# Kernel optimization log

Hardware: AMD Instinct MI355X
Metric: run time of the kernel (lower is better)

Reference implementation:

```python
import jax, jax.numpy as jnp
import numpy as np

B, S, D, H = 2, 2048, 1024, 16
DK = D // H

def setup_inputs() -> dict:
    key = jax.random.key(0)
    ks = jax.random.split(key, 12)
    def lin(k, shape, fan_in):
        bound = 1.0 / np.sqrt(fan_in)
        return jax.random.uniform(k, shape, jnp.float32, -bound, bound)
    inp = {
        'Q': jax.random.normal(ks[0], (B, S, D), jnp.float32),
        'K': jax.random.normal(ks[1], (B, S, D), jnp.float32),
        'V': jax.random.normal(ks[2], (B, S, D), jnp.float32),
        # padding mask: last 128 key positions of batch element 0 are padding
        'padding_mask': jnp.ones((B, 1, 1, S), jnp.int32).at[0, :, :, -128:].set(0),
        # causal look-ahead mask
        'look_ahead_mask': jnp.tril(jnp.ones((S, S), jnp.int32))[None, None],
        'Wq': lin(ks[3], (D, D), D), 'bq': lin(ks[4], (D,), D),
        'Wk': lin(ks[5], (D, D), D), 'bk': lin(ks[6], (D,), D),
        'Wv': lin(ks[7], (D, D), D), 'bv': lin(ks[8], (D,), D),
        'Wo': lin(ks[9], (D, D), D), 'bo': lin(ks[10], (D,), D),
    }
    return inp

def _split_heads(x):
    # [B,S,D] -> [B,H,S,DK]
    b, s, _ = x.shape
    return x.reshape(b, s, H, DK).transpose(0, 2, 1, 3)

def reference(Q, K, V, padding_mask, look_ahead_mask, Wq, bq, Wk, bk, Wv, bv, Wo, bo):
    q = _split_heads(Q @ Wq.T + bq)  # [B,H,S,DK]
    k = _split_heads(K @ Wk.T + bk)
    v = _split_heads(V @ Wv.T + bv)
    scores = jnp.einsum('bhqd,bhkd->bhqk', q, k) / np.sqrt(DK).astype(np.float32)
    neg_inf = jnp.float32(-jnp.inf)
    scores = jnp.where(padding_mask == 0, neg_inf, scores)
    scores = jnp.where(look_ahead_mask == 0, neg_inf, scores)
    weights = jax.nn.softmax(scores, axis=-1)  # dropout is identity in eval mode
    x = jnp.einsum('bhqk,bhkd->bhqd', weights, v)  # [B,H,S,DK]
    x = x.transpose(0, 2, 1, 3).reshape(Q.shape[0], Q.shape[1], D)
    return x @ Wo.T + bo
```

## Files before the change

kernel.cpp:

```cpp
#include <hip/hip_runtime.h>
#include <hip/hip_bf16.h>

#define B_   2
#define S_   2048
#define D_   1024
#define H_   16
#define DK_  64

typedef unsigned short u16;
typedef __attribute__((ext_vector_type(8))) short bf16x8;
typedef __attribute__((ext_vector_type(4))) float f32x4;

static __device__ __forceinline__ u16 f2bf(float f) {
  union { float f; unsigned u; } v; v.f = f;
  unsigned r = v.u + 0x7FFF + ((v.u >> 16) & 1);
  return (u16)(r >> 16);
}

static __device__ __forceinline__ void gl_lds16(const void* g, void* l) {
  __builtin_amdgcn_global_load_lds(
      (const __attribute__((address_space(1))) void*)g,
      (__attribute__((address_space(3))) void*)l, 16, 0, 0);
}

__global__ void cvt3(const float4* __restrict__ a, const float4* __restrict__ b, const float4* __restrict__ c,
                     ushort4* __restrict__ oa, ushort4* __restrict__ ob, ushort4* __restrict__ oc, int n4) {
  int y = blockIdx.y;
  const float4* in = (y == 0) ? a : (y == 1) ? b : c;
  ushort4* out = (y == 0) ? oa : (y == 1) ? ob : oc;
  int i = blockIdx.x * blockDim.x + threadIdx.x;
  if (i < n4) {
    float4 v = in[i];
    ushort4 r;
    r.x = f2bf(v.x); r.y = f2bf(v.y); r.z = f2bf(v.z); r.w = f2bf(v.w);
    out[i] = r;
  }
}
__global__ void cvt4(const float4* __restrict__ a, const float4* __restrict__ b, const float4* __restrict__ c,
                     const float4* __restrict__ d, ushort4* __restrict__ oa, ushort4* __restrict__ ob,
                     ushort4* __restrict__ oc, ushort4* __restrict__ od, int n4) {
  int y = blockIdx.y;
  const float4* in = (y == 0) ? a : (y == 1) ? b : (y == 2) ? c : d;
  ushort4* out = (y == 0) ? oa : (y == 1) ? ob : (y == 2) ? oc : od;
  int i = blockIdx.x * blockDim.x + threadIdx.x;
  if (i < n4) {
    float4 v = in[i];
    ushort4 r;
    r.x = f2bf(v.x); r.y = f2bf(v.y); r.z = f2bf(v.z); r.w = f2bf(v.w);
    out[i] = r;
  }
}

__launch_bounds__(256, 2)
__global__ void gemm_qkv(const u16* __restrict__ Xq, const u16* __restrict__ Xk, const u16* __restrict__ Xv,
                         const u16* __restrict__ Wq, const u16* __restrict__ Wk, const u16* __restrict__ Wv,
                         const float* __restrict__ bq, const float* __restrict__ bk, const float* __restrict__ bv,
                         u16* __restrict__ outq, u16* __restrict__ outk, u16* __restrict__ outv) {
  const int z = blockIdx.z;
  const u16* Am; const u16* Bm; int m0, n0;
  if (z == 2) { Am = Wv; Bm = Xv; m0 = blockIdx.x * 128; n0 = blockIdx.y * 128; }
  else if (z == 1) { Am = Xk; Bm = Wk; m0 = blockIdx.y * 128; n0 = blockIdx.x * 128; }
  else { Am = Xq; Bm = Wq; m0 = blockIdx.y * 128; n0 = blockIdx.x * 128; }
  const float* bias = (z == 0) ? bq : (z == 1) ? bk : bv;

  __shared__ __align__(16) u16 As[128 * 32];
  __shared__ __align__(16) u16 Bs[128 * 32];

  const int tid = threadIdx.x, lane = tid & 63, w = tid >> 6;
  const int q = lane >> 4, cl = lane & 15;
  const int wr = w >> 1, wc = w & 1;

  f32x4 acc[4][4] = {};

  for (int k0 = 0; k0 < D_; k0 += 32) {
#pragma unroll
    for (int i = 0; i < 2; ++i) {
      int cb = (i * 4 + w) * 64;
      int ch = cb + lane;
      int row = ch >> 2, ko = (ch & 3) << 3;
      gl_lds16(Am + (size_t)(m0 + row) * D_ + k0 + ko, As + cb * 8);
      gl_lds16(Bm + (size_t)(n0 + row) * D_ + k0 + ko, Bs + cb * 8);
    }
    __syncthreads();

    bf16x8 af[4], bfr[4];
#pragma unroll
    for (int r = 0; r < 4; ++r) af[r]  = *(const bf16x8*)(As + (wr * 64 + r * 16 + cl) * 32 + q * 8);
#pragma unroll
    for (int c = 0; c < 4; ++c) bfr[c] = *(const bf16x8*)(Bs + (wc * 64 + c * 16 + cl) * 32 + q * 8);
#pragma unroll
    for (int r = 0; r < 4; ++r)
#pragma unroll
      for (int c = 0; c < 4; ++c)
        acc[r][c] = __builtin_amdgcn_mfma_f32_16x16x32_bf16(af[r], bfr[c], acc[r][c], 0, 0, 0);
    __syncthreads();
  }

  if (z == 2) {
#pragma unroll
    for (int r = 0; r < 4; ++r) {
#pragma unroll
      for (int rr = 0; rr < 4; ++rr) {
        int j = m0 + wr * 64 + r * 16 + q * 4 + rr;
        float bval = bias[j];
        int hh = j >> 6, dk = j & 63;
#pragma unroll
        for (int c = 0; c < 4; ++c) {
          int n = n0 + wc * 64 + c * 16 + cl;
          int bb = n >> 11, s = n & (S_ - 1);
          outv[((size_t)(bb * H_ + hh) * DK_ + dk) * S_ + s] = f2bf(acc[r][c][rr] + bval);
        }
      }
    }
  } else {
    const float scale = (z == 0) ? 0.125f : 1.0f;
    u16* o = (z == 0) ? outq : outk;
#pragma unroll
    for (int c = 0; c < 4; ++c) {
      int j = n0 + wc * 64 + c * 16 + cl;
      float bval = bias[j];
      int hh = j >> 6, dk = j & 63;
#pragma unroll
      for (int r = 0; r < 4; ++r) {
#pragma unroll
        for (int rr = 0; rr < 4; ++rr) {
          int n = m0 + wr * 64 + r * 16 + q * 4 + rr;
          int bb = n >> 11, s = n & (S_ - 1);
          o[((size_t)(bb * H_ + hh) * S_ + s) * DK_ + dk] = f2bf((acc[r][c][rr] + bval) * scale);
        }
      }
    }
  }
}

__launch_bounds__(256, 2)
__global__ void attn(const u16* __restrict__ qh, const u16* __restrict__ kh,
                     const u16* __restrict__ vt, const int* __restrict__ pad,
                     u16* __restrict__ attn_out) {
  __shared__ __align__(16) u16 Ks[64 * 64];
  __shared__ __align__(16) u16 Vs[64 * 64];
  __shared__ __align__(16) u16 Ps[4][16 * 72];
  __shared__ float Kbias[64];

  const int tid = threadIdx.x, lane = tid & 63, w = tid >> 6;
  const int q = lane >> 4, cl = lane & 15;
  const int qt = (int)gridDim.x - 1 - (int)blockIdx.x;
  const int qb = qt * 64, h = blockIdx.y, b = blockIdx.z;

  const u16* Q = qh + (size_t)(b * H_ + h) * S_ * DK_;
  const u16* K = kh + (size_t)(b * H_ + h) * S_ * DK_;
  const u16* V = vt + (size_t)(b * H_ + h) * DK_ * S_;
  const int* pm = pad + b * S_;

  const int qr0 = qb + w * 16;
  bf16x8 qf0 = *(const bf16x8*)(Q + (qr0 + cl) * DK_ + q * 8);
  bf16x8 qf1 = *(const bf16x8*)(Q + (qr0 + cl) * DK_ + 32 + q * 8);

  f32x4 o[4] = {};
  float ls[4] = {0.f, 0.f, 0.f, 0.f};
  u16* Pw = Ps[w];

  const int nkv = qt + 1;
  for (int it = 0; it < nkv; ++it) {
    const int kb = it << 6;
#pragma unroll
    for (int i = 0; i < 2; ++i) {
      int s = (i * 4 + w) * 64 + lane;
      int row = s >> 3;
      int c = (s & 7) ^ (row & 7);
      gl_lds16(K + (size_t)(kb + row) * DK_ + (c << 3), Ks + (size_t)s * 8);
      gl_lds16(V + (size_t)row * S_ + kb + (c << 3), Vs + (size_t)s * 8);
    }
    if (tid < 64) {
      Kbias[tid] = (pm[kb + tid] != 0) ? -6.0f : -3e38f;
    }
    __syncthreads();

    f32x4 sa[4];
#pragma unroll
    for (int ct = 0; ct < 4; ++ct) {
      int rk = ct * 16 + cl;
      int c0 = q ^ (rk & 7);
      bf16x8 kf0 = *(const bf16x8*)(Ks + rk * 64 + (c0 << 3));
      bf16x8 kf1 = *(const bf16x8*)(Ks + rk * 64 + ((c0 ^ 4) << 3));
      f32x4 zz = {};
      zz = __builtin_amdgcn_mfma_f32_16x16x32_bf16(qf0, kf0, zz, 0, 0, 0);
      zz = __builtin_amdgcn_mfma_f32_16x16x32_bf16(qf1, kf1, zz, 0, 0, 0);
      sa[ct] = zz;
    }

    if (it < qt) {
#pragma unroll
      for (int ct = 0; ct < 4; ++ct) {
        float kbv = Kbias[ct * 16 + cl];
#pragma unroll
        for (int rr = 0; rr < 4; ++rr) {
          float p = __expf(sa[ct][rr] + kbv);
          ls[rr] += p;
          Pw[(q * 4 + rr) * 72 + ct * 16 + cl] = f2bf(p);
        }
      }
    } else {
#pragma unroll
      for (int ct = 0; ct < 4; ++ct) {
        int kg = kb + ct * 16 + cl;
        float kbv = Kbias[ct * 16 + cl];
#pragma unroll
        for (int rr = 0; rr < 4; ++rr) {
          int qg = qr0 + q * 4 + rr;
          float p = (kg <= qg) ? __expf(sa[ct][rr] + kbv) : 0.f;
          ls[rr] += p;
          Pw[(q * 4 + rr) * 72 + ct * 16 + cl] = f2bf(p);
        }
      }
    }

    bf16x8 pf0 = *(const bf16x8*)(Pw + cl * 72 + q * 8);
    bf16x8 pf1 = *(const bf16x8*)(Pw + cl * 72 + 32 + q * 8);

#pragma unroll
    for (int ct = 0; ct < 4; ++ct) {
      int rv = ct * 16 + cl;
      int c0 = q ^ (rv & 7);
      bf16x8 vf0 = *(const bf16x8*)(Vs + rv * 64 + (c0 << 3));
      bf16x8 vf1 = *(const bf16x8*)(Vs + rv * 64 + ((c0 ^ 4) << 3));
      o[ct] = __builtin_amdgcn_mfma_f32_16x16x32_bf16(pf0, vf0, o[ct], 0, 0, 0);
      o[ct] = __builtin_amdgcn_mfma_f32_16x16x32_bf16(pf1, vf1, o[ct], 0, 0, 0);
    }
    __syncthreads();
  }

#pragma unroll
  for (int rr = 0; rr < 4; ++rr) {
    float l = ls[rr];
    l += __shfl_xor(l, 1, 64);
    l += __shfl_xor(l, 2, 64);
    l += __shfl_xor(l, 4, 64);
    l += __shfl_xor(l, 8, 64);
    float inv = 1.0f / l;
    int qg = qr0 + q * 4 + rr;
    size_t base = (size_t)(b * S_ + qg) * D_ + h * DK_;
#pragma unroll
    for (int ct = 0; ct < 4; ++ct)
      attn_out[base + ct * 16 + cl] = f2bf(o[ct][rr] * inv);
  }
}

__launch_bounds__(256, 2)
__global__ void gemm_out(const u16* __restrict__ A, const u16* __restrict__ W,
                         const float* __restrict__ bias, float* __restrict__ out) {
  __shared__ __align__(16) u16 As[128 * 32];
  __shared__ __align__(16) u16 Bs[128 * 32];

  const int tid = threadIdx.x, lane = tid & 63, w = tid >> 6;
  const int q = lane >> 4, cl = lane & 15;
  const int wr = w >> 1, wc = w & 1;
  const int m0 = blockIdx.y * 128, n0 = blockIdx.x * 128;

  f32x4 acc[4][4] = {};

  for (int k0 = 0; k0 < D_; k0 += 32) {
#pragma unroll
    for (int i = 0; i < 2; ++i) {
      int cb = (i * 4 + w) * 64;
      int ch = cb + lane;
      int row = ch >> 2, ko = (ch & 3) << 3;
      gl_lds16(A + (size_t)(m0 + row) * D_ + k0 + ko, As + cb * 8);
      gl_lds16(W + (size_t)(n0 + row) * D_ + k0 + ko, Bs + cb * 8);
    }
    __syncthreads();

    bf16x8 af[4], bfr[4];
#pragma unroll
    for (int r = 0; r < 4; ++r) af[r]  = *(const bf16x8*)(As + (wr * 64 + r * 16 + cl) * 32 + q * 8);
#pragma unroll
    for (int c = 0; c < 4; ++c) bfr[c] = *(const bf16x8*)(Bs + (wc * 64 + c * 16 + cl) * 32 + q * 8);
#pragma unroll
    for (int r = 0; r < 4; ++r)
#pragma unroll
      for (int c = 0; c < 4; ++c)
        acc[r][c] = __builtin_amdgcn_mfma_f32_16x16x32_bf16(af[r], bfr[c], acc[r][c], 0, 0, 0);
    __syncthreads();
  }

#pragma unroll
  for (int c = 0; c < 4; ++c) {
    int j = n0 + wc * 64 + c * 16 + cl;
    float bval = bias[j];
#pragma unroll
    for (int r = 0; r < 4; ++r) {
#pragma unroll
      for (int rr = 0; rr < 4; ++rr) {
        int n = m0 + wr * 64 + r * 16 + q * 4 + rr;
        out[(size_t)n * D_ + j] = acc[r][c][rr] + bval;
      }
    }
  }
}

extern "C" void kernel_launch(void* const* d_in, const int* in_sizes, int n_in,
                              void* d_out, int out_size, void* d_ws, size_t ws_size,
                              hipStream_t stream) {
  const float* Qf  = (const float*)d_in[0];
  const float* Kf  = (const float*)d_in[1];
  const float* Vf  = (const float*)d_in[2];
  const int*   pad = (const int*)d_in[3];
  const float* Wqf = (const float*)d_in[5];
  const float* bq  = (const float*)d_in[6];
  const float* Wkf = (const float*)d_in[7];
  const float* bk  = (const float*)d_in[8];
  const float* Wvf = (const float*)d_in[9];
  const float* bv  = (const float*)d_in[10];
  const float* Wof = (const float*)d_in[11];
  const float* bo  = (const float*)d_in[12];

  const size_t BSD = (size_t)B_ * S_ * D_;
  const size_t DD  = (size_t)D_ * D_;

  char* ws = (char*)d_ws;
  u16* Qb   = (u16*)ws; ws += BSD * 2;
  u16* Kb   = (u16*)ws; ws += BSD * 2;
  u16* Vb   = (u16*)ws; ws += BSD * 2;
  u16* Wqb  = (u16*)ws; ws += DD * 2;
  u16* Wkb  = (u16*)ws; ws += DD * 2;
  u16* Wvb  = (u16*)ws; ws += DD * 2;
  u16* Wob  = (u16*)ws; ws += DD * 2;
  u16* qhd  = (u16*)ws; ws += BSD * 2;
  u16* khd  = (u16*)ws; ws += BSD * 2;
  u16* vtd  = (u16*)ws; ws += BSD * 2;
  u16* attn_o = (u16*)ws; ws += BSD * 2;

  const int n4 = (int)(BSD / 4);
  const int w4 = (int)(DD / 4);
  dim3 gc3(n4 / 256, 3), gc4(w4 / 256, 4);
  cvt3<<<gc3, 256, 0, stream>>>((const float4*)Qf, (const float4*)Kf, (const float4*)Vf,
                                (ushort4*)Qb, (ushort4*)Kb, (ushort4*)Vb, n4);
  cvt4<<<gc4, 256, 0, stream>>>((const float4*)Wqf, (const float4*)Wkf, (const float4*)Wvf, (const float4*)Wof,
                                (ushort4*)Wqb, (ushort4*)Wkb, (ushort4*)Wvb, (ushort4*)Wob, w4);

  dim3 g1(D_ / 128, (B_ * S_) / 128, 3);
  gemm_qkv<<<g1, 256, 0, stream>>>(Qb, Kb, Vb, Wqb, Wkb, Wvb, bq, bk, bv, qhd, khd, vtd);

  dim3 g2(S_ / 64, H_, B_);
  attn<<<g2, 256, 0, stream>>>(qhd, khd, vtd, pad, attn_o);

  dim3 g3(D_ / 128, (B_ * S_) / 128);
  gemm_out<<<g3, 256, 0, stream>>>(attn_o, Wob, bo, (float*)d_out);
}
```

Baseline: 258.5 us.

## Load K/V fragments directly from global memory, dropping LDS staging and barriers

```diff
diff --git a/kernel.cpp b/kernel.cpp
--- a/kernel.cpp
+++ b/kernel.cpp
@@ -133,14 +133,11 @@
   }
 }
 
-__launch_bounds__(256, 2)
+__launch_bounds__(256, 4)
 __global__ void attn(const u16* __restrict__ qh, const u16* __restrict__ kh,
                      const u16* __restrict__ vt, const int* __restrict__ pad,
                      u16* __restrict__ attn_out) {
-  __shared__ __align__(16) u16 Ks[64 * 64];
-  __shared__ __align__(16) u16 Vs[64 * 64];
   __shared__ __align__(16) u16 Ps[4][16 * 72];
-  __shared__ float Kbias[64];
 
   const int tid = threadIdx.x, lane = tid & 63, w = tid >> 6;
   const int q = lane >> 4, cl = lane & 15;
@@ -163,26 +160,18 @@
   const int nkv = qt + 1;
   for (int it = 0; it < nkv; ++it) {
     const int kb = it << 6;
-#pragma unroll
-    for (int i = 0; i < 2; ++i) {
-      int s = (i * 4 + w) * 64 + lane;
-      int row = s >> 3;
-      int c = (s & 7) ^ (row & 7);
-      gl_lds16(K + (size_t)(kb + row) * DK_ + (c << 3), Ks + (size_t)s * 8);
-      gl_lds16(V + (size_t)row * S_ + kb + (c << 3), Vs + (size_t)s * 8);
-    }
-    if (tid < 64) {
-      Kbias[tid] = (pm[kb + tid] != 0) ? -6.0f : -3e38f;
-    }
-    __syncthreads();
+
+    float kbv[4];
+#pragma unroll
+    for (int ct = 0; ct < 4; ++ct)
+      kbv[ct] = (pm[kb + ct * 16 + cl] != 0) ? -6.0f : -3e38f;
 
     f32x4 sa[4];
 #pragma unroll
     for (int ct = 0; ct < 4; ++ct) {
-      int rk = ct * 16 + cl;
-      int c0 = q ^ (rk & 7);
-      bf16x8 kf0 = *(const bf16x8*)(Ks + rk * 64 + (c0 << 3));
-      bf16x8 kf1 = *(const bf16x8*)(Ks + rk * 64 + ((c0 ^ 4) << 3));
+      const u16* Kr = K + (size_t)(kb + ct * 16 + cl) * DK_;
+      bf16x8 kf0 = *(const bf16x8*)(Kr + q * 8);
+      bf16x8 kf1 = *(const bf16x8*)(Kr + 32 + q * 8);
       f32x4 zz = {};
       zz = __builtin_amdgcn_mfma_f32_16x16x32_bf16(qf0, kf0, zz, 0, 0, 0);
       zz = __builtin_amdgcn_mfma_f32_16x16x32_bf16(qf1, kf1, zz, 0, 0, 0);
@@ -192,10 +181,9 @@
     if (it < qt) {
 #pragma unroll
       for (int ct = 0; ct < 4; ++ct) {
-        float kbv = Kbias[ct * 16 + cl];
 #pragma unroll
         for (int rr = 0; rr < 4; ++rr) {
-          float p = __expf(sa[ct][rr] + kbv);
+          float p = __expf(sa[ct][rr] + kbv[ct]);
           ls[rr] += p;
           Pw[(q * 4 + rr) * 72 + ct * 16 + cl] = f2bf(p);
         }
@@ -204,11 +192,10 @@
 #pragma unroll
       for (int ct = 0; ct < 4; ++ct) {
         int kg = kb + ct * 16 + cl;
-        float kbv = Kbias[ct * 16 + cl];
 #pragma unroll
         for (int rr = 0; rr < 4; ++rr) {
           int qg = qr0 + q * 4 + rr;
-          float p = (kg <= qg) ? __expf(sa[ct][rr] + kbv) : 0.f;
+          float p = (kg <= qg) ? __expf(sa[ct][rr] + kbv[ct]) : 0.f;
           ls[rr] += p;
           Pw[(q * 4 + rr) * 72 + ct * 16 + cl] = f2bf(p);
         }
@@ -220,14 +207,12 @@
 
 #pragma unroll
     for (int ct = 0; ct < 4; ++ct) {
-      int rv = ct * 16 + cl;
-      int c0 = q ^ (rv & 7);
-      bf16x8 vf0 = *(const bf16x8*)(Vs + rv * 64 + (c0 << 3));
-      bf16x8 vf1 = *(const bf16x8*)(Vs + rv * 64 + ((c0 ^ 4) << 3));
+      const u16* Vr = V + (size_t)(ct * 16 + cl) * S_ + kb;
+      bf16x8 vf0 = *(const bf16x8*)(Vr + q * 8);
+      bf16x8 vf1 = *(const bf16x8*)(Vr + 32 + q * 8);
       o[ct] = __builtin_amdgcn_mfma_f32_16x16x32_bf16(pf0, vf0, o[ct], 0, 0, 0);
       o[ct] = __builtin_amdgcn_mfma_f32_16x16x32_bf16(pf1, vf1, o[ct], 0, 0, 0);
     }
-    __syncthreads();
   }
 
 #pragma unroll
```

New measurement: 428.2 us. +65.6%, slower.

## Split long causal KV ranges into chunks with a separate combine kernel

Applied to the files above, without the earlier changes.

```diff
diff --git a/kernel.cpp b/kernel.cpp
--- a/kernel.cpp
+++ b/kernel.cpp
@@ -11,6 +11,9 @@
 typedef __attribute__((ext_vector_type(8))) short bf16x8;
 typedef __attribute__((ext_vector_type(4))) float f32x4;
 
+#define CHUNK_   12
+#define NSLOT_   48
+
 static __device__ __forceinline__ u16 f2bf(float f) {
   union { float f; unsigned u; } v; v.f = f;
   unsigned r = v.u + 0x7FFF + ((v.u >> 16) & 1);
@@ -23,27 +26,27 @@
       (__attribute__((address_space(3))) void*)l, 16, 0, 0);
 }
 
-__global__ void cvt3(const float4* __restrict__ a, const float4* __restrict__ b, const float4* __restrict__ c,
-                     ushort4* __restrict__ oa, ushort4* __restrict__ ob, ushort4* __restrict__ oc, int n4) {
+__global__ void cvt7(const float4* __restrict__ i0, const float4* __restrict__ i1,
+                     const float4* __restrict__ i2, const float4* __restrict__ i3,
+                     const float4* __restrict__ i4, const float4* __restrict__ i5,
+                     const float4* __restrict__ i6,
+                     ushort4* __restrict__ o0, ushort4* __restrict__ o1,
+                     ushort4* __restrict__ o2, ushort4* __restrict__ o3,
+                     ushort4* __restrict__ o4, ushort4* __restrict__ o5,
+                     ushort4* __restrict__ o6, int nbig, int nsmall) {
   int y = blockIdx.y;
-  const float4* in = (y == 0) ? a : (y == 1) ? b : c;
-  ushort4* out = (y == 0) ? oa : (y == 1) ? ob : oc;
+  const float4* in; ushort4* out; int bound;
+  switch (y) {
+    case 0: in = i0; out = o0; bound = nbig; break;
+    case 1: in = i1; out = o1; bound = nbig; break;
+    case 2: in = i2; out = o2; bound = nbig; break;
+    case 3: in = i3; out = o3; bound = nsmall; break;
+    case 4: in = i4; out = o4; bound = nsmall; break;
+    case 5: in = i5; out = o5; bound = nsmall; break;
+    default: in = i6; out = o6; bound = nsmall; break;
+  }
   int i = blockIdx.x * blockDim.x + threadIdx.x;
-  if (i < n4) {
-    float4 v = in[i];
-    ushort4 r;
-    r.x = f2bf(v.x); r.y = f2bf(v.y); r.z = f2bf(v.z); r.w = f2bf(v.w);
-    out[i] = r;
-  }
-}
-__global__ void cvt4(const float4* __restrict__ a, const float4* __restrict__ b, const float4* __restrict__ c,
-                     const float4* __restrict__ d, ushort4* __restrict__ oa, ushort4* __restrict__ ob,
-                     ushort4* __restrict__ oc, ushort4* __restrict__ od, int n4) {
-  int y = blockIdx.y;
-  const float4* in = (y == 0) ? a : (y == 1) ? b : (y == 2) ? c : d;
-  ushort4* out = (y == 0) ? oa : (y == 1) ? ob : (y == 2) ? oc : od;
-  int i = blockIdx.x * blockDim.x + threadIdx.x;
-  if (i < n4) {
+  if (i < bound) {
     float4 v = in[i];
     ushort4 r;
     r.x = f2bf(v.x); r.y = f2bf(v.y); r.z = f2bf(v.z); r.w = f2bf(v.w);
@@ -133,10 +136,10 @@
   }
 }
 
-__launch_bounds__(256, 2)
+__launch_bounds__(256, 4)
 __global__ void attn(const u16* __restrict__ qh, const u16* __restrict__ kh,
                      const u16* __restrict__ vt, const int* __restrict__ pad,
-                     u16* __restrict__ attn_out) {
+                     u16* __restrict__ attn_out, float* __restrict__ Po, float* __restrict__ Pl) {
   __shared__ __align__(16) u16 Ks[64 * 64];
   __shared__ __align__(16) u16 Vs[64 * 64];
   __shared__ __align__(16) u16 Ps[4][16 * 72];
@@ -144,8 +147,16 @@
 
   const int tid = threadIdx.x, lane = tid & 63, w = tid >> 6;
   const int q = lane >> 4, cl = lane & 15;
-  const int qt = (int)gridDim.x - 1 - (int)blockIdx.x;
-  const int qb = qt * 64, h = blockIdx.y, b = blockIdx.z;
+  const int h = blockIdx.y, b = blockIdx.z;
+
+  const int x = blockIdx.x;
+  int qt, ch, nch;
+  if (x < 24)      { qt = 24 + x / 3;          ch = x % 3;       nch = 3; }
+  else if (x < 48) { int y = x - 24; qt = 12 + y / 2; ch = y & 1; nch = 2; }
+  else             { qt = x - 48;              ch = 0;           nch = 1; }
+  const int qb = qt * 64;
+  const int t0 = ch * CHUNK_;
+  const int t1 = (qt < t0 + CHUNK_ - 1) ? qt : (t0 + CHUNK_ - 1);
 
   const u16* Q = qh + (size_t)(b * H_ + h) * S_ * DK_;
   const u16* K = kh + (size_t)(b * H_ + h) * S_ * DK_;
@@ -160,8 +171,7 @@
   float ls[4] = {0.f, 0.f, 0.f, 0.f};
   u16* Pw = Ps[w];
 
-  const int nkv = qt + 1;
-  for (int it = 0; it < nkv; ++it) {
+  for (int it = t0; it <= t1; ++it) {
     const int kb = it << 6;
 #pragma unroll
     for (int i = 0; i < 2; ++i) {
@@ -230,19 +240,62 @@
     __syncthreads();
   }
 
-#pragma unroll
-  for (int rr = 0; rr < 4; ++rr) {
-    float l = ls[rr];
-    l += __shfl_xor(l, 1, 64);
-    l += __shfl_xor(l, 2, 64);
-    l += __shfl_xor(l, 4, 64);
-    l += __shfl_xor(l, 8, 64);
-    float inv = 1.0f / l;
-    int qg = qr0 + q * 4 + rr;
-    size_t base = (size_t)(b * S_ + qg) * D_ + h * DK_;
-#pragma unroll
-    for (int ct = 0; ct < 4; ++ct)
-      attn_out[base + ct * 16 + cl] = f2bf(o[ct][rr] * inv);
+  if (nch == 1) {
+#pragma unroll
+    for (int rr = 0; rr < 4; ++rr) {
+      float l = ls[rr];
+      l += __shfl_xor(l, 1, 64);
+      l += __shfl_xor(l, 2, 64);
+      l += __shfl_xor(l, 4, 64);
+      l += __shfl_xor(l, 8, 64);
+      float inv = 1.0f / l;
+      int qg = qr0 + q * 4 + rr;
+      size_t base = (size_t)(b * S_ + qg) * D_ + h * DK_;
+#pragma unroll
+      for (int ct = 0; ct < 4; ++ct)
+        attn_out[base + ct * 16 + cl] = f2bf(o[ct][rr] * inv);
+    }
+  } else {
+    int pq = qt - 12;
+    int off = (pq < 12) ? pq * 2 : 24 + (pq - 12) * 3;
+    size_t slot = (size_t)(b * H_ + h) * NSLOT_ + off + ch;
+#pragma unroll
+    for (int rr = 0; rr < 4; ++rr) {
+      float l = ls[rr];
+      l += __shfl_xor(l, 1, 64);
+      l += __shfl_xor(l, 2, 64);
+      l += __shfl_xor(l, 4, 64);
+      l += __shfl_xor(l, 8, 64);
+      int rl = w * 16 + q * 4 + rr;
+      if (cl == 0) Pl[slot * 64 + rl] = l;
+      float* po = Po + ((size_t)slot * 64 + rl) * 64;
+#pragma unroll
+      for (int ct = 0; ct < 4; ++ct)
+        po[ct * 16 + cl] = o[ct][rr];
+    }
+  }
+}
+
+__global__ void combine(const float* __restrict__ Po, const float* __restrict__ Pl,
+                        u16* __restrict__ attn_out) {
+  const int qt = 12 + blockIdx.x, h = blockIdx.y, b = blockIdx.z;
+  const int nch = (qt < 24) ? 2 : 3;
+  const int pq = qt - 12;
+  const int off = (pq < 12) ? pq * 2 : 24 + (pq - 12) * 3;
+  const size_t slot0 = (size_t)(b * H_ + h) * NSLOT_ + off;
+
+  const int c = threadIdx.x & 63;
+  const int r0 = (threadIdx.x >> 6) * 16;
+#pragma unroll 4
+  for (int i = 0; i < 16; ++i) {
+    int r = r0 + i;
+    float os = 0.f, lsum = 0.f;
+    for (int ch = 0; ch < nch; ++ch) {
+      os += Po[((slot0 + ch) * 64 + r) * 64 + c];
+      lsum += Pl[(slot0 + ch) * 64 + r];
+    }
+    int qg = qt * 64 + r;
+    attn_out[(size_t)(b * S_ + qg) * D_ + h * DK_ + c] = f2bf(os / lsum);
   }
 }
 
@@ -330,19 +383,25 @@
   u16* vtd  = (u16*)ws; ws += BSD * 2;
   u16* attn_o = (u16*)ws; ws += BSD * 2;
 
+  float* Po = (float*)d_ws;
+  float* Pl = Po + (size_t)B_ * H_ * NSLOT_ * 64 * 64;
+
   const int n4 = (int)(BSD / 4);
   const int w4 = (int)(DD / 4);
-  dim3 gc3(n4 / 256, 3), gc4(w4 / 256, 4);
-  cvt3<<<gc3, 256, 0, stream>>>((const float4*)Qf, (const float4*)Kf, (const float4*)Vf,
-                                (ushort4*)Qb, (ushort4*)Kb, (ushort4*)Vb, n4);
-  cvt4<<<gc4, 256, 0, stream>>>((const float4*)Wqf, (const float4*)Wkf, (const float4*)Wvf, (const float4*)Wof,
-                                (ushort4*)Wqb, (ushort4*)Wkb, (ushort4*)Wvb, (ushort4*)Wob, w4);
+  dim3 gc(n4 / 256, 7);
+  cvt7<<<gc, 256, 0, stream>>>((const float4*)Qf, (const float4*)Kf, (const float4*)Vf,
+                               (const float4*)Wqf, (const float4*)Wkf, (const float4*)Wvf, (const float4*)Wof,
+                               (ushort4*)Qb, (ushort4*)Kb, (ushort4*)Vb,
+                               (ushort4*)Wqb, (ushort4*)Wkb, (ushort4*)Wvb, (ushort4*)Wob, n4, w4);
 
   dim3 g1(D_ / 128, (B_ * S_) / 128, 3);
   gemm_qkv<<<g1, 256, 0, stream>>>(Qb, Kb, Vb, Wqb, Wkb, Wvb, bq, bk, bv, qhd, khd, vtd);
 
-  dim3 g2(S_ / 64, H_, B_);
-  attn<<<g2, 256, 0, stream>>>(qhd, khd, vtd, pad, attn_o);
+  dim3 g2(60, H_, B_);
+  attn<<<g2, 256, 0, stream>>>(qhd, khd, vtd, pad, attn_o, Po, Pl);
+
+  dim3 g2b(20, H_, B_);
+  combine<<<g2b, 256, 0, stream>>>(Po, Pl, attn_o);
 
   dim3 g3(D_ / 128, (B_ * S_) / 128);
   gemm_out<<<g3, 256, 0, stream>>>(attn_o, Wob, bo, (float*)d_out);
```

Result: no change. 257.5 us (-0.4%).
